# Kernel tuning notes

Measured on AMD Instinct MI355X. Metric: run time of the kernel, lower is better.

The kernel has to match this reference:

```python
import jax, jax.numpy as jnp
import numpy as np

NUM_WIRES = 12   # qubits -> 2**12 = 4096 amplitudes
N_LAYERS = 4
BATCH = 8192


def setup_inputs() -> dict:
    key = jax.random.key(0)
    k1, k2, k3 = jax.random.split(key, 3)
    return {
        "state_batch": jax.random.normal(k1, (BATCH, NUM_WIRES), dtype=jnp.float32),
        "params": jax.random.normal(k2, (NUM_WIRES,), dtype=jnp.float32),
        "head_w": jax.random.normal(k3, (1, NUM_WIRES), dtype=jnp.float32) / np.sqrt(NUM_WIRES),
        "head_b": jnp.zeros((1,), dtype=jnp.float32),
    }


# --- batched real-valued statevector simulator (RY/CNOT are real matrices) ---

def _apply_ry_per_sample(psi, theta, w):
    # psi: (B, 2**n), theta: (B,) per-sample angle on wire w
    B = psi.shape[0]
    s = psi.reshape(B, 2 ** w, 2, -1)          # (B, L, 2, R)
    c, si = jnp.cos(theta * 0.5), jnp.sin(theta * 0.5)
    M = jnp.stack([jnp.stack([c, -si], -1), jnp.stack([si, c], -1)], -2)  # (B,2,2)
    s = jnp.einsum('bij,bljr->blir', M, s)
    return s.reshape(B, -1)


def _apply_ry_shared(psi, theta, w):
    # theta: scalar shared angle on wire w
    B = psi.shape[0]
    s = psi.reshape(B, 2 ** w, 2, -1)
    c, si = jnp.cos(theta * 0.5), jnp.sin(theta * 0.5)
    M = jnp.stack([jnp.stack([c, -si]), jnp.stack([si, c])])  # (2,2)
    s = jnp.einsum('ij,bljr->blir', M, s)
    return s.reshape(B, -1)


def _apply_cnot(psi, w):
    # CNOT on (control=w, target=w+1), adjacent wires
    B = psi.shape[0]
    s = psi.reshape(B, 2 ** w, 2, 2, -1)       # (B, L, ctrl, tgt, R)
    s = jnp.stack([s[:, :, 0], s[:, :, 1, ::-1]], axis=2)  # flip target where ctrl=1
    return s.reshape(B, -1)


def _pauliz_expval(probs, w):
    # probs: (B, 2**n) real probabilities; <Z_w> = P(wire w = 0) - P(wire w = 1)
    B = probs.shape[0]
    p = probs.reshape(B, 2 ** w, 2, -1)
    return p[:, :, 0].sum(axis=(1, 2)) - p[:, :, 1].sum(axis=(1, 2))


def reference(state_batch, params, head_w, head_b):
    B, n = state_batch.shape
    # |0...0> initial state
    psi = jnp.zeros((B, 2 ** n), dtype=state_batch.dtype).at[:, 0].set(1.0)
    # encoding layer: RY(state[i]) on each wire (batched over samples)
    for w in range(n):
        psi = _apply_ry_per_sample(psi, state_batch[:, w], w)
    # variational layers: CNOT ladder then shared-param RY on each wire
    for _ in range(N_LAYERS):
        for w in range(n - 1):
            psi = _apply_cnot(psi, w)
        for w in range(n):
            psi = _apply_ry_shared(psi, params[w], w)
    probs = psi * psi  # real amplitudes -> probabilities
    exps = jnp.stack([_pauliz_expval(probs, w) for w in range(n)], axis=-1)  # (B, n)
    return (exps @ head_w.T + head_b).squeeze(-1)  # (B,)
```

## Files before the change

### kernel.cpp

```cpp
#include <hip/hip_runtime.h>


constexpr unsigned pair_mask(int t, int w) {
    unsigned m = 0;
    for (int d = 0; w + d < 12; ++d)
        if ((d & ~(unsigned)t) == 0) m |= 1u << (w + d);
    return m;
}
constexpr unsigned side_mask(int t, int w) {
    unsigned s = 16u - (unsigned)t;
    unsigned m = 0;
    for (int d = 0; d <= w; ++d)
        if (((unsigned)d & ~s) == 0) m |= 1u << (w - d);
    return m;
}
constexpr unsigned z_mask(int w) {
    unsigned m = 0;
    for (int u = w; u >= 0; u -= 4) m |= 1u << u;
    return m;
}

static_assert(pair_mask(1, 0) == 0b11u, "");
static_assert(pair_mask(2, 3) == ((1u << 3) | (1u << 5)), "");
static_assert(pair_mask(4, 7) == ((1u << 7) | (1u << 11)), "");
static_assert(side_mask(1, 2) == 0b111u, "");
static_assert(side_mask(4, 11) == ((1u << 11) | (1u << 7) | (1u << 3)), "");
static_assert(z_mask(9) == ((1u << 9) | (1u << 5) | (1u << 1)), "");

template <unsigned LM, unsigned RM, unsigned SL, unsigned SR>
__device__ __forceinline__ void ry(float (&v)[64], float c, float s, unsigned lane) {
    const float ss = (__popc(SL & lane) & 1) ? s : -s;
    if constexpr (RM == 0u) {
#pragma unroll
        for (int r = 0; r < 64; ++r) {
            float p = __shfl_xor(v[r], (int)LM, 64);
            float t = p * ss;
            v[r] = (__builtin_popcount(SR & (unsigned)r) & 1) ? fmaf(c, v[r], -t)
                                                              : fmaf(c, v[r], t);
        }
    } else {
#pragma unroll
        for (int r = 0; r < 64; ++r) {
            const int r2 = r ^ (int)RM;
            if (r > r2) continue;
            float a = v[r], b = v[r2];
            float pa = (LM != 0u) ? __shfl_xor(b, (int)LM, 64) : b;
            float pb = (LM != 0u) ? __shfl_xor(a, (int)LM, 64) : a;
            float ta = pa * ss, tb = pb * ss;
            v[r]  = (__builtin_popcount(SR & (unsigned)r)  & 1) ? fmaf(c, a, -ta)
                                                                : fmaf(c, a, ta);
            v[r2] = (__builtin_popcount(SR & (unsigned)r2) & 1) ? fmaf(c, b, -tb)
                                                                : fmaf(c, b, tb);
        }
    }
}

#define RY_APPLY(T, W)                                                              \
    ry<(pair_mask(T, W) & 63u), (pair_mask(T, W) >> 6), (side_mask(T, W) & 63u),    \
       (side_mask(T, W) >> 6)>(v, cpar[W], spar[W], lane);

#define LAYER(T)                                                      \
    RY_APPLY(T, 0) RY_APPLY(T, 1) RY_APPLY(T, 2) RY_APPLY(T, 3)       \
    RY_APPLY(T, 4) RY_APPLY(T, 5) RY_APPLY(T, 6) RY_APPLY(T, 7)       \
    RY_APPLY(T, 8) RY_APPLY(T, 9) RY_APPLY(T, 10) RY_APPLY(T, 11)

__global__ void __launch_bounds__(256) qnn12_kernel(
    const float* __restrict__ state, const float* __restrict__ params,
    const float* __restrict__ head_w, const float* __restrict__ head_b,
    float* __restrict__ out, int B) {
    __shared__ float Wt[4096];

    const int tid = threadIdx.x;
    const unsigned lane = (unsigned)(tid & 63);
    const int wid = tid >> 6;
    const int sample = blockIdx.x * 4 + wid;
    const bool active = sample < B;

    {
        float hwv[12];
#pragma unroll
        for (int w = 0; w < 12; ++w) hwv[w] = head_w[w];
#pragma unroll
        for (int k = 0; k < 16; ++k) {
            int i = tid + (k << 8);
            float a = 0.f;
#pragma unroll
            for (int w = 0; w < 12; ++w)
                a += (__builtin_popcount(z_mask(w) & (unsigned)i) & 1) ? -hwv[w] : hwv[w];
            Wt[i] = a;
        }
    }
    __syncthreads();

    float ang = 0.f;
    if (active && lane < 12u) ang = state[sample * 12 + (int)lane];
    else if (lane >= 16u && lane < 28u) ang = params[lane - 16u];
    float sv_, cv_;
    __sincosf(0.5f * ang, &sv_, &cv_);

    float cpar[12], spar[12];
#pragma unroll
    for (int w = 0; w < 12; ++w) {
        cpar[w] = __shfl(cv_, 16 + w, 64);
        spar[w] = __shfl(sv_, 16 + w, 64);
    }

    float pre = 1.f;
#pragma unroll
    for (int w = 0; w < 6; ++w) {
        float cw = __shfl(cv_, w, 64), sw = __shfl(sv_, w, 64);
        pre *= ((lane >> w) & 1u) ? sw : cw;
    }
    float fc[6], fs[6];
#pragma unroll
    for (int i = 0; i < 6; ++i) {
        fc[i] = __shfl(cv_, 6 + i, 64);
        fs[i] = __shfl(sv_, 6 + i, 64);
    }

    float v[64];
    {
        float t4[16];
#pragma unroll
        for (int j = 0; j < 16; ++j) {
            float x = pre;
            x *= (j & 1) ? fs[0] : fc[0];
            x *= (j & 2) ? fs[1] : fc[1];
            x *= (j & 4) ? fs[2] : fc[2];
            x *= (j & 8) ? fs[3] : fc[3];
            t4[j] = x;
        }
#pragma unroll
        for (int r = 0; r < 64; ++r) {
            float x = t4[r & 15];
            x *= ((r >> 4) & 1) ? fs[4] : fc[4];
            x *= ((r >> 5) & 1) ? fs[5] : fc[5];
            v[r] = x;
        }
    }

    LAYER(1)
    LAYER(2)
    LAYER(3)
    LAYER(4)

    float a0 = 0.f, a1 = 0.f, a2 = 0.f, a3 = 0.f;
#pragma unroll
    for (int r = 0; r < 64; r += 4) {
        float w0 = Wt[((r + 0) << 6) + (int)lane];
        float w1 = Wt[((r + 1) << 6) + (int)lane];
        float w2 = Wt[((r + 2) << 6) + (int)lane];
        float w3 = Wt[((r + 3) << 6) + (int)lane];
        a0 = fmaf(v[r + 0] * w0, v[r + 0], a0);
        a1 = fmaf(v[r + 1] * w1, v[r + 1], a1);
        a2 = fmaf(v[r + 2] * w2, v[r + 2], a2);
        a3 = fmaf(v[r + 3] * w3, v[r + 3], a3);
    }
    float acc = (a0 + a1) + (a2 + a3);
#pragma unroll
    for (int off = 32; off > 0; off >>= 1) acc += __shfl_xor(acc, off, 64);

    if (active && lane == 0u) out[sample] = acc + head_b[0];
}

extern "C" void kernel_launch(void* const* d_in, const int* in_sizes, int n_in,
                              void* d_out, int out_size, void* d_ws, size_t ws_size,
                              hipStream_t stream) {
    const float* state  = (const float*)d_in[0];
    const float* params = (const float*)d_in[1];
    const float* head_w = (const float*)d_in[2];
    const float* head_b = (const float*)d_in[3];
    float* out = (float*)d_out;

    const int B = in_sizes[0] / 12;
    const int blocks = (B + 3) / 4;
    hipLaunchKernelGGL(qnn12_kernel, dim3(blocks), dim3(256), 0, stream,
                       state, params, head_w, head_b, out, B);
}
```

Measured before the change: 202.5 us.

## Split each sample's statevector across two wavefronts with LDS exchange for wire-0 gate

```diff
diff --git a/kernel.cpp b/kernel.cpp
--- a/kernel.cpp
+++ b/kernel.cpp
@@ -26,21 +26,25 @@
 static_assert(side_mask(1, 2) == 0b111u, "");
 static_assert(side_mask(4, 11) == ((1u << 11) | (1u << 7) | (1u << 3)), "");
 static_assert(z_mask(9) == ((1u << 9) | (1u << 5) | (1u << 1)), "");
+static_assert((pair_mask(1, 0) >> 7) == 0u && (pair_mask(2, 0) >> 7) == 0u, "");
+static_assert((pair_mask(3, 0) >> 7) == 0u && (pair_mask(4, 0) >> 7) == 0u, "");
+static_assert((pair_mask(3, 1) & 1u) == 0u && (pair_mask(4, 5) & 1u) == 0u, "");
 
-template <unsigned LM, unsigned RM, unsigned SL, unsigned SR>
-__device__ __forceinline__ void ry(float (&v)[64], float c, float s, unsigned lane) {
-    const float ss = (__popc(SL & lane) & 1) ? s : -s;
+template <unsigned LM, unsigned RM, unsigned SW, unsigned SL, unsigned SR>
+__device__ __forceinline__ void ry32(float (&v)[32], float c, float s,
+                                     unsigned lane, unsigned p) {
+    const float ss = (((unsigned)__popc(SL & lane) ^ (SW & p)) & 1u) ? s : -s;
     if constexpr (RM == 0u) {
 #pragma unroll
-        for (int r = 0; r < 64; ++r) {
-            float p = __shfl_xor(v[r], (int)LM, 64);
-            float t = p * ss;
+        for (int r = 0; r < 32; ++r) {
+            float pv = __shfl_xor(v[r], (int)LM, 64);
+            float t = pv * ss;
             v[r] = (__builtin_popcount(SR & (unsigned)r) & 1) ? fmaf(c, v[r], -t)
                                                               : fmaf(c, v[r], t);
         }
     } else {
 #pragma unroll
-        for (int r = 0; r < 64; ++r) {
+        for (int r = 0; r < 32; ++r) {
             const int r2 = r ^ (int)RM;
             if (r > r2) continue;
             float a = v[r], b = v[r2];
@@ -55,42 +59,52 @@
     }
 }
 
-#define RY_APPLY(T, W)                                                              \
-    ry<(pair_mask(T, W) & 63u), (pair_mask(T, W) >> 6), (side_mask(T, W) & 63u),    \
-       (side_mask(T, W) >> 6)>(v, cpar[W], spar[W], lane);
+#define RY_APPLY(T, W)                                                         \
+    {                                                                          \
+        const float c_ = __shfl(cv_, 16 + (W), 64);                            \
+        const float s_ = __shfl(sv_, 16 + (W), 64);                            \
+        ry32<((pair_mask(T, W) >> 1) & 63u), (pair_mask(T, W) >> 7),           \
+             (side_mask(T, W) & 1u), ((side_mask(T, W) >> 1) & 63u),           \
+             (side_mask(T, W) >> 7)>(v, c_, s_, lane, p);                      \
+    }
 
-#define LAYER(T)                                                      \
-    RY_APPLY(T, 0) RY_APPLY(T, 1) RY_APPLY(T, 2) RY_APPLY(T, 3)       \
-    RY_APPLY(T, 4) RY_APPLY(T, 5) RY_APPLY(T, 6) RY_APPLY(T, 7)       \
-    RY_APPLY(T, 8) RY_APPLY(T, 9) RY_APPLY(T, 10) RY_APPLY(T, 11)
+#define XGATE(T)                                                               \
+    {                                                                          \
+        const float c_ = __shfl(cv_, 16, 64);                                  \
+        const float s_ = __shfl(sv_, 16, 64);                                  \
+        const float ss = p ? s_ : -s_;                                         \
+        constexpr unsigned ML = (pair_mask(T, 0) >> 1) & 63u;                  \
+        _Pragma("unroll") for (int h = 0; h < 2; ++h) {                        \
+            _Pragma("unroll") for (int cc = 0; cc < 16; ++cc)                  \
+                xb[pr][p][cc][lane] = v[h * 16 + cc];                          \
+            __syncthreads();                                                   \
+            _Pragma("unroll") for (int cc = 0; cc < 16; ++cc) {                \
+                float pv = xb[pr][p ^ 1u][cc][lane ^ ML];                      \
+                v[h * 16 + cc] = fmaf(c_, v[h * 16 + cc], ss * pv);            \
+            }                                                                  \
+            __syncthreads();                                                   \
+        }                                                                      \
+    }
+
+#define LAYER(T)                                                               \
+    XGATE(T)                                                                   \
+    RY_APPLY(T, 1) RY_APPLY(T, 2) RY_APPLY(T, 3) RY_APPLY(T, 4)                \
+    RY_APPLY(T, 5) RY_APPLY(T, 6) RY_APPLY(T, 7) RY_APPLY(T, 8)                \
+    RY_APPLY(T, 9) RY_APPLY(T, 10) RY_APPLY(T, 11)
 
 __global__ void __launch_bounds__(256) qnn12_kernel(
     const float* __restrict__ state, const float* __restrict__ params,
     const float* __restrict__ head_w, const float* __restrict__ head_b,
     float* __restrict__ out, int B) {
-    __shared__ float Wt[4096];
+    __shared__ float xb[2][2][16][64];
 
     const int tid = threadIdx.x;
     const unsigned lane = (unsigned)(tid & 63);
     const int wid = tid >> 6;
-    const int sample = blockIdx.x * 4 + wid;
+    const int pr = wid >> 1;
+    const unsigned p = (unsigned)(wid & 1);
+    const int sample = blockIdx.x * 2 + pr;
     const bool active = sample < B;
-
-    {
-        float hwv[12];
-#pragma unroll
-        for (int w = 0; w < 12; ++w) hwv[w] = head_w[w];
-#pragma unroll
-        for (int k = 0; k < 16; ++k) {
-            int i = tid + (k << 8);
-            float a = 0.f;
-#pragma unroll
-            for (int w = 0; w < 12; ++w)
-                a += (__builtin_popcount(z_mask(w) & (unsigned)i) & 1) ? -hwv[w] : hwv[w];
-            Wt[i] = a;
-        }
-    }
-    __syncthreads();
 
     float ang = 0.f;
     if (active && lane < 12u) ang = state[sample * 12 + (int)lane];
@@ -98,27 +112,24 @@
     float sv_, cv_;
     __sincosf(0.5f * ang, &sv_, &cv_);
 
-    float cpar[12], spar[12];
+    float pre;
+    {
+        float c0 = __shfl(cv_, 0, 64), s0 = __shfl(sv_, 0, 64);
+        pre = p ? s0 : c0;
+    }
 #pragma unroll
-    for (int w = 0; w < 12; ++w) {
-        cpar[w] = __shfl(cv_, 16 + w, 64);
-        spar[w] = __shfl(sv_, 16 + w, 64);
+    for (int j = 0; j < 6; ++j) {
+        float cw = __shfl(cv_, 1 + j, 64), sw = __shfl(sv_, 1 + j, 64);
+        pre *= ((lane >> j) & 1u) ? sw : cw;
+    }
+    float fc[5], fs[5];
+#pragma unroll
+    for (int k = 0; k < 5; ++k) {
+        fc[k] = __shfl(cv_, 7 + k, 64);
+        fs[k] = __shfl(sv_, 7 + k, 64);
     }
 
-    float pre = 1.f;
-#pragma unroll
-    for (int w = 0; w < 6; ++w) {
-        float cw = __shfl(cv_, w, 64), sw = __shfl(sv_, w, 64);
-        pre *= ((lane >> w) & 1u) ? sw : cw;
-    }
-    float fc[6], fs[6];
-#pragma unroll
-    for (int i = 0; i < 6; ++i) {
-        fc[i] = __shfl(cv_, 6 + i, 64);
-        fs[i] = __shfl(sv_, 6 + i, 64);
-    }
-
-    float v[64];
+    float v[32];
     {
         float t4[16];
 #pragma unroll
@@ -131,12 +142,8 @@
             t4[j] = x;
         }
 #pragma unroll
-        for (int r = 0; r < 64; ++r) {
-            float x = t4[r & 15];
-            x *= ((r >> 4) & 1) ? fs[4] : fc[4];
-            x *= ((r >> 5) & 1) ? fs[5] : fc[5];
-            v[r] = x;
-        }
+        for (int r = 0; r < 32; ++r)
+            v[r] = t4[r & 15] * ((r & 16) ? fs[4] : fc[4]);
     }
 
     LAYER(1)
@@ -144,23 +151,36 @@
     LAYER(3)
     LAYER(4)
 
-    float a0 = 0.f, a1 = 0.f, a2 = 0.f, a3 = 0.f;
+    float a[12];
 #pragma unroll
-    for (int r = 0; r < 64; r += 4) {
-        float w0 = Wt[((r + 0) << 6) + (int)lane];
-        float w1 = Wt[((r + 1) << 6) + (int)lane];
-        float w2 = Wt[((r + 2) << 6) + (int)lane];
-        float w3 = Wt[((r + 3) << 6) + (int)lane];
-        a0 = fmaf(v[r + 0] * w0, v[r + 0], a0);
-        a1 = fmaf(v[r + 1] * w1, v[r + 1], a1);
-        a2 = fmaf(v[r + 2] * w2, v[r + 2], a2);
-        a3 = fmaf(v[r + 3] * w3, v[r + 3], a3);
+    for (int w = 0; w < 12; ++w) {
+        const unsigned z = z_mask(w);
+        const unsigned zl = (z >> 1) & 63u, zw = z & 1u;
+        const int sgn = (int)(((unsigned)__popc(zl & lane) ^ (zw & p)) & 1u);
+        const float h = head_w[w];
+        a[w] = sgn ? -h : h;
     }
-    float acc = (a0 + a1) + (a2 + a3);
+    const float A0 = ((a[0] + a[1]) + (a[2] + a[3])) + ((a[4] + a[5]) + a[6]);
+
+    float acc = 0.f;
+#pragma unroll
+    for (int r = 0; r < 32; ++r) {
+        float wr = A0;
+        wr += (__builtin_popcount((z_mask(7) >> 7) & (unsigned)r) & 1) ? -a[7] : a[7];
+        wr += (__builtin_popcount((z_mask(8) >> 7) & (unsigned)r) & 1) ? -a[8] : a[8];
+        wr += (__builtin_popcount((z_mask(9) >> 7) & (unsigned)r) & 1) ? -a[9] : a[9];
+        wr += (__builtin_popcount((z_mask(10) >> 7) & (unsigned)r) & 1) ? -a[10] : a[10];
+        wr += (__builtin_popcount((z_mask(11) >> 7) & (unsigned)r) & 1) ? -a[11] : a[11];
+        acc = fmaf(v[r] * wr, v[r], acc);
+    }
 #pragma unroll
     for (int off = 32; off > 0; off >>= 1) acc += __shfl_xor(acc, off, 64);
 
-    if (active && lane == 0u) out[sample] = acc + head_b[0];
+    float* red = &xb[0][0][0][0];
+    if (lane == 0u) red[wid] = acc;
+    __syncthreads();
+    if (active && p == 0u && lane == 0u)
+        out[sample] = red[wid] + red[wid | 1] + head_b[0];
 }
 
 extern "C" void kernel_launch(void* const* d_in, const int* in_sizes, int n_in,
@@ -173,7 +193,7 @@
     float* out = (float*)d_out;
 
     const int B = in_sizes[0] / 12;
-    const int blocks = (B + 3) / 4;
+    const int blocks = (B + 1) / 2;
     hipLaunchKernelGGL(qnn12_kernel, dim3(blocks), dim3(256), 0, stream,
                        state, params, head_w, head_b, out, B);
 }
```

After: 217.5 us. +7.4%, slower.
